# Kernel optimization log

Hardware: AMD Instinct MI355X
Metric: run time of the kernel (lower is better)

The kernel has to match this reference:

```python
import jax, jax.numpy as jnp
import numpy as np

MARGIN = 40.0


def setup_inputs() -> dict:
    key = jax.random.key(0)
    k1, k2 = jax.random.split(key)
    feat = jax.random.normal(k1, (4096, 512), dtype=jnp.float32)
    targets = jax.random.randint(k2, (4096,), 0, 64, dtype=jnp.int64)
    return {"feat": feat, "targets": targets}


def reference(feat, targets):
    # corr: (n, n) Gram matrix of features
    corr = feat @ feat.T
    # mask[i, j] = True if same class
    mask = targets[:, None] == targets[None, :]
    big = jnp.asarray(jnp.finfo(corr.dtype).max, corr.dtype)
    # per-row min over positives, max over negatives
    corr_ap = jnp.min(jnp.where(mask, corr, big), axis=1)
    corr_an = jnp.max(jnp.where(mask, -big, corr), axis=1)
    # MarginRankingLoss(margin=40) with y = 1: mean(relu(-(ap - an) + margin))
    loss = jnp.mean(jax.nn.relu(corr_an - corr_ap + MARGIN))
    return loss
```

## Files before the change

kernel.cpp:

```cpp
#include <hip/hip_runtime.h>
#include <float.h>
#include <stdint.h>


#define N_ROWS 4096
#define D_K    512
#define BT     128
#define NKB    (D_K / 16)
#define NTB    (N_ROWS / BT)
#define NTILES (NTB * (NTB + 1) / 2)
#define MARGIN 40.0f
#define FOLD_BLOCKS 16
#define RBLK   (32 * 64 * 8)

typedef __bf16 bf16_t;
typedef bf16_t bf16x8 __attribute__((ext_vector_type(8)));
typedef bf16_t bf16x4 __attribute__((ext_vector_type(4)));
typedef float  floatx16 __attribute__((ext_vector_type(16)));
typedef unsigned short ushort_t;

__device__ __forceinline__ ushort_t f2bf_rne(float x) {
    uint32_t u = __builtin_bit_cast(uint32_t, x);
    return (ushort_t)((u + 0x7FFFu + ((u >> 16) & 1u)) >> 16);
}

__global__ __launch_bounds__(256) void cast_kernel(
    const float* __restrict__ f, ushort_t* __restrict__ fbp,
    int* __restrict__ counter)
{
    __shared__ __align__(16) ushort_t lds[32 * 512];
    const int R   = blockIdx.x;
    const int tid = threadIdx.x;
    if (R == 0 && tid == 0) *counter = 0;

#pragma unroll
    for (int p = 0; p < 16; ++p) {
        const int fi   = p * 256 + tid;
        const int row  = fi >> 7;
        const int col4 = fi & 127;
        const float4 v = *(const float4*)(f + ((size_t)(R * 32 + row) << 9) + col4 * 4);
        bf16x4 o;
        o[0] = __builtin_bit_cast(bf16_t, f2bf_rne(v.x));
        o[1] = __builtin_bit_cast(bf16_t, f2bf_rne(v.y));
        o[2] = __builtin_bit_cast(bf16_t, f2bf_rne(v.z));
        o[3] = __builtin_bit_cast(bf16_t, f2bf_rne(v.w));
        const int chunk = (col4 >> 1) ^ (row & 7);
        *(bf16x4*)(lds + row * 512 + chunk * 8 + (col4 & 1) * 4) = o;
    }
    __syncthreads();

#pragma unroll
    for (int p = 0; p < 8; ++p) {
        const int c  = p * 256 + tid;
        const int l  = c & 63;
        const int r  = l & 31;
        const int lc = ((c >> 6) * 2 + (l >> 5)) ^ (r & 7);
        const bf16x8 val = *(const bf16x8*)(lds + r * 512 + lc * 8);
        *(bf16x8*)(fbp + (size_t)R * RBLK + (size_t)c * 8) = val;
    }
}

#define MFMA4()                                                               \
    do {                                                                      \
        acc[0][0] = __builtin_amdgcn_mfma_f32_32x32x16_bf16(a0, b0, acc[0][0], 0, 0, 0); \
        acc[0][1] = __builtin_amdgcn_mfma_f32_32x32x16_bf16(a0, b1, acc[0][1], 0, 0, 0); \
        acc[1][0] = __builtin_amdgcn_mfma_f32_32x32x16_bf16(a1, b0, acc[1][0], 0, 0, 0); \
        acc[1][1] = __builtin_amdgcn_mfma_f32_32x32x16_bf16(a1, b1, acc[1][1], 0, 0, 0); \
    } while (0)

__global__ __launch_bounds__(256, 4) void gram_mfma_kernel(
    const ushort_t* __restrict__ fbp, const int* __restrict__ tgt,
    float* __restrict__ ap_part, float* __restrict__ an_part)
{
    __shared__ int tgI[BT];
    __shared__ int tgJ[BT];
    __shared__ float apRed[2 * BT], anRed[2 * BT];
    __shared__ float apRedT[2 * BT], anRedT[2 * BT];

    int bi = 0, rem = blockIdx.x;
    while (rem >= NTB - bi) { rem -= NTB - bi; ++bi; }
    const int bj = bi + rem;

    const int tid  = threadIdx.x;
    const int i0   = bi * BT;
    const int j0   = bj * BT;
    const int lane = tid & 63;
    const int wave = tid >> 6;
    const int wr   = wave >> 1;
    const int wc   = wave & 1;
    const int cl   = lane & 31;
    const int hh   = lane >> 5;

    if (tid < BT) tgI[tid] = tgt[i0 + tid];
    else          tgJ[tid - BT] = tgt[j0 + tid - BT];
    __syncthreads();

    const ushort_t* pA = fbp + (size_t)(bi * 4 + wr * 2) * RBLK + lane * 8;
    const ushort_t* pB = fbp + (size_t)(bj * 4 + wc * 2) * RBLK + lane * 8;

    floatx16 acc[2][2];
#pragma unroll
    for (int a = 0; a < 2; ++a)
#pragma unroll
        for (int b = 0; b < 2; ++b) acc[a][b] = (floatx16)0.0f;

    bf16x8 a0 = *(const bf16x8*)(pA);
    bf16x8 a1 = *(const bf16x8*)(pA + RBLK);
    bf16x8 b0 = *(const bf16x8*)(pB);
    bf16x8 b1 = *(const bf16x8*)(pB + RBLK);

#pragma unroll 4
    for (int kb = 0; kb < NKB - 1; ++kb) {
        const int o = (kb + 1) * 512;
        const bf16x8 na0 = *(const bf16x8*)(pA + o);
        const bf16x8 na1 = *(const bf16x8*)(pA + RBLK + o);
        const bf16x8 nb0 = *(const bf16x8*)(pB + o);
        const bf16x8 nb1 = *(const bf16x8*)(pB + RBLK + o);
        MFMA4();
        a0 = na0; a1 = na1; b0 = nb0; b1 = nb1;
    }
    MFMA4();

    const int tj0 = tgJ[wc * 64 + cl];
    const int tj1 = tgJ[wc * 64 + 32 + cl];

    float apT[2], anT[2];
#pragma unroll
    for (int cg = 0; cg < 2; ++cg) { apT[cg] = FLT_MAX; anT[cg] = -FLT_MAX; }

#pragma unroll
    for (int rg = 0; rg < 2; ++rg) {
        const int rbase = wr * 64 + rg * 32 + 4 * hh;
#pragma unroll
        for (int reg = 0; reg < 16; ++reg) {
            const int row = rbase + (reg & 3) + 8 * (reg >> 2);
            const int ti = tgI[row];
            const float v0 = acc[rg][0][reg];
            const float v1 = acc[rg][1][reg];
            float vap = FLT_MAX, van = -FLT_MAX;
            if (ti == tj0) { vap = fminf(vap, v0); apT[0] = fminf(apT[0], v0); }
            else           { van = fmaxf(van, v0); anT[0] = fmaxf(anT[0], v0); }
            if (ti == tj1) { vap = fminf(vap, v1); apT[1] = fminf(apT[1], v1); }
            else           { van = fmaxf(van, v1); anT[1] = fmaxf(anT[1], v1); }
#pragma unroll
            for (int m = 1; m < 32; m <<= 1) {
                vap = fminf(vap, __shfl_xor(vap, m));
                van = fmaxf(van, __shfl_xor(van, m));
            }
            if (cl == 0) {
                apRed[wc * BT + row] = vap;
                anRed[wc * BT + row] = van;
            }
        }
    }
#pragma unroll
    for (int cg = 0; cg < 2; ++cg) {
        float vap = apT[cg], van = anT[cg];
        vap = fminf(vap, __shfl_xor(vap, 32));
        van = fmaxf(van, __shfl_xor(van, 32));
        if (lane < 32) {
            apRedT[wr * BT + wc * 64 + cg * 32 + cl] = vap;
            anRedT[wr * BT + wc * 64 + cg * 32 + cl] = van;
        }
    }
    __syncthreads();

    if (tid < BT) {
        ap_part[(size_t)bj * N_ROWS + i0 + tid] =
            fminf(apRed[tid], apRed[BT + tid]);
        an_part[(size_t)bj * N_ROWS + i0 + tid] =
            fmaxf(anRed[tid], anRed[BT + tid]);
        if (bi != bj) {
            ap_part[(size_t)bi * N_ROWS + j0 + tid] =
                fminf(apRedT[tid], apRedT[BT + tid]);
            an_part[(size_t)bi * N_ROWS + j0 + tid] =
                fmaxf(anRedT[tid], anRedT[BT + tid]);
        }
    }
}

__global__ __launch_bounds__(256) void fold_kernel(
    const float* __restrict__ ap_part, const float* __restrict__ an_part,
    float* __restrict__ blk_sum, int* __restrict__ counter,
    float* __restrict__ out)
{
    __shared__ float sred[4];
    const int tid = threadIdx.x;
    const int row = blockIdx.x * 256 + tid;
    const int lane = tid & 63;
    const int wave = tid >> 6;

    float ap = FLT_MAX, an = -FLT_MAX;
#pragma unroll 8
    for (int s = 0; s < NTB; ++s) {
        ap = fminf(ap, ap_part[(size_t)s * N_ROWS + row]);
        an = fmaxf(an, an_part[(size_t)s * N_ROWS + row]);
    }
    const float v = an - ap + MARGIN;
    float local = (v > 0.0f) ? v : 0.0f;
#pragma unroll
    for (int m = 32; m >= 1; m >>= 1) local += __shfl_down(local, m);
    if (lane == 0) sred[wave] = local;
    __syncthreads();

    if (tid == 0) {
        blk_sum[blockIdx.x] = sred[0] + sred[1] + sred[2] + sred[3];
        __threadfence();
        if (atomicAdd(counter, 1) == FOLD_BLOCKS - 1) {
            __threadfence();
            float s = 0.0f;
#pragma unroll
            for (int b = 0; b < FOLD_BLOCKS; ++b) s += blk_sum[b];
            out[0] = s * (1.0f / N_ROWS);
        }
    }
}

extern "C" void kernel_launch(void* const* d_in, const int* in_sizes, int n_in,
                              void* d_out, int out_size, void* d_ws, size_t ws_size,
                              hipStream_t stream)
{
    const float* feat = (const float*)d_in[0];
    const int*   tgt  = (const int*)d_in[1];

    ushort_t* fbp     = (ushort_t*)d_ws;
    float*    ap_part = (float*)(fbp + (size_t)N_ROWS * D_K);
    float*    an_part = ap_part + (size_t)NTB * N_ROWS;
    float*    blk_sum = an_part + (size_t)NTB * N_ROWS;
    int*      counter = (int*)(blk_sum + FOLD_BLOCKS);

    cast_kernel<<<N_ROWS / 32, 256, 0, stream>>>(feat, fbp, counter);
    gram_mfma_kernel<<<NTILES, 256, 0, stream>>>(fbp, tgt, ap_part, an_part);
    fold_kernel<<<FOLD_BLOCKS, 256, 0, stream>>>(ap_part, an_part, blk_sum,
                                                 counter, (float*)d_out);
}
```

Baseline: 92.28 us.

## Double-buffer global fragment loads in bursts of two k-steps in Gram kernel

Replaces the single-step register prefetch in the MFMA main loop with two register buffers, each holding two k-steps of A/B fragments, loaded in alternating bursts so more global loads are in flight during MFMA work. The launch-bounds occupancy hint drops from 4 to 3 blocks per SM to leave room for the extra registers. The change trades occupancy for deeper per-wave memory-level parallelism.

```diff
diff --git a/kernel.cpp b/kernel.cpp
--- a/kernel.cpp
+++ b/kernel.cpp
@@ -6,7 +6,6 @@
 #define N_ROWS 4096
 #define D_K    512
 #define BT     128
-#define NKB    (D_K / 16)
 #define NTB    (N_ROWS / BT)
 #define NTILES (NTB * (NTB + 1) / 2)
 #define MARGIN 40.0f
@@ -60,15 +59,7 @@
     }
 }
 
-#define MFMA4()                                                               \
-    do {                                                                      \
-        acc[0][0] = __builtin_amdgcn_mfma_f32_32x32x16_bf16(a0, b0, acc[0][0], 0, 0, 0); \
-        acc[0][1] = __builtin_amdgcn_mfma_f32_32x32x16_bf16(a0, b1, acc[0][1], 0, 0, 0); \
-        acc[1][0] = __builtin_amdgcn_mfma_f32_32x32x16_bf16(a1, b0, acc[1][0], 0, 0, 0); \
-        acc[1][1] = __builtin_amdgcn_mfma_f32_32x32x16_bf16(a1, b1, acc[1][1], 0, 0, 0); \
-    } while (0)
-
-__global__ __launch_bounds__(256, 4) void gram_mfma_kernel(
+__global__ __launch_bounds__(256, 3) void gram_mfma_kernel(
     const ushort_t* __restrict__ fbp, const int* __restrict__ tgt,
     float* __restrict__ ap_part, float* __restrict__ an_part)
 {
@@ -104,22 +95,41 @@
 #pragma unroll
         for (int b = 0; b < 2; ++b) acc[a][b] = (floatx16)0.0f;
 
-    bf16x8 a0 = *(const bf16x8*)(pA);
-    bf16x8 a1 = *(const bf16x8*)(pA + RBLK);
-    bf16x8 b0 = *(const bf16x8*)(pB);
-    bf16x8 b1 = *(const bf16x8*)(pB + RBLK);
-
-#pragma unroll 4
-    for (int kb = 0; kb < NKB - 1; ++kb) {
-        const int o = (kb + 1) * 512;
-        const bf16x8 na0 = *(const bf16x8*)(pA + o);
-        const bf16x8 na1 = *(const bf16x8*)(pA + RBLK + o);
-        const bf16x8 nb0 = *(const bf16x8*)(pB + o);
-        const bf16x8 nb1 = *(const bf16x8*)(pB + RBLK + o);
-        MFMA4();
-        a0 = na0; a1 = na1; b0 = nb0; b1 = nb1;
-    }
-    MFMA4();
+    bf16x8 F[2][4], G[2][4];
+
+#define LOAD_BURST(dst, burst)                                                \
+    do {                                                                      \
+        const int _o = (burst) * 1024;                                        \
+        _Pragma("unroll")                                                     \
+        for (int q = 0; q < 2; ++q) {                                         \
+            dst[q][0] = *(const bf16x8*)(pA + _o + q * 512);                  \
+            dst[q][1] = *(const bf16x8*)(pA + RBLK + _o + q * 512);           \
+            dst[q][2] = *(const bf16x8*)(pB + _o + q * 512);                  \
+            dst[q][3] = *(const bf16x8*)(pB + RBLK + _o + q * 512);           \
+        }                                                                     \
+    } while (0)
+
+#define COMPUTE_BURST(src)                                                    \
+    do {                                                                      \
+        _Pragma("unroll")                                                     \
+        for (int q = 0; q < 2; ++q) {                                         \
+            acc[0][0] = __builtin_amdgcn_mfma_f32_32x32x16_bf16(src[q][0], src[q][2], acc[0][0], 0, 0, 0); \
+            acc[0][1] = __builtin_amdgcn_mfma_f32_32x32x16_bf16(src[q][0], src[q][3], acc[0][1], 0, 0, 0); \
+            acc[1][0] = __builtin_amdgcn_mfma_f32_32x32x16_bf16(src[q][1], src[q][2], acc[1][0], 0, 0, 0); \
+            acc[1][1] = __builtin_amdgcn_mfma_f32_32x32x16_bf16(src[q][1], src[q][3], acc[1][1], 0, 0, 0); \
+        }                                                                     \
+    } while (0)
+
+    LOAD_BURST(F, 0);
+    LOAD_BURST(G, 1);
+    for (int it = 0; it < 7; ++it) {
+        COMPUTE_BURST(F);
+        LOAD_BURST(F, 2 * it + 2);
+        COMPUTE_BURST(G);
+        LOAD_BURST(G, 2 * it + 3);
+    }
+    COMPUTE_BURST(F);
+    COMPUTE_BURST(G);
 
     const int tj0 = tgJ[wc * 64 + cl];
     const int tj1 = tgJ[wc * 64 + 32 + cl];
```

Result: no change. 94.08 us (+1.9%).
